# Performance work log

Hardware: AMD Instinct MI355X
Metric: run time of the kernel (lower is better)

The kernel has to match this reference:

```python
import jax, jax.numpy as jnp
import numpy as np

N_TRIALS, T, INPUT_DIM = 32, 512, 64
N, R, OUTPUT_DIM = 4096, 8, 64
DT = 0.1


def setup_inputs() -> dict:
    key = jax.random.key(0)
    k_inp, k_B, k_W, k_m, k_n = jax.random.split(key, 5)
    inp = jax.random.normal(k_inp, (N_TRIALS, T, INPUT_DIM), dtype=jnp.float32)
    B = jax.random.normal(k_B, (N, INPUT_DIM), dtype=jnp.float32)
    W = jax.random.normal(k_W, (OUTPUT_DIM, N), dtype=jnp.float32) / np.sqrt(N)
    m = jax.random.normal(k_m, (N, R), dtype=jnp.float32)
    n = jax.random.normal(k_n, (N, R), dtype=jnp.float32)
    return {"inp": inp, "B": B, "W": W, "m": m, "n": n}


def reference(inp, B, W, m, n):
    # inp: [b, t, i]; B: [N, i]; W: [o, N]; m, n: [N, r]
    n_trials = inp.shape[0]
    # Precompute input projection for all steps: [t, b, N]
    inp_proj = jnp.einsum('bti,ni->tbn', inp, B)

    def step(x, u):
        # x: [b, N] voltage; u: [b, N] projected input at this step
        # sigmoid(x) @ (m n^T / N)^T == ((sigmoid(x) @ n) @ m^T) / N
        rec = (jax.nn.sigmoid(x) @ n) @ m.T / N
        x_new = (1.0 - DT) * x + DT * (rec + u)
        y = jax.nn.sigmoid(x_new) @ W.T  # [b, o]
        return x_new, (x_new, y)

    x0 = jnp.zeros((n_trials, N), dtype=inp.dtype)
    _, (xs, ys) = jax.lax.scan(step, x0, inp_proj)
    # xs: [t, b, N]; ys: [t, b, o]
    x_seq = jnp.concatenate([x0[None], xs], axis=0).transpose(1, 0, 2)  # [b, t+1, N]
    output_seq = ys.transpose(1, 0, 2)  # [b, t, o]
    return (x_seq, output_seq)
```

## Files before the change

### kernel.cpp

```cpp
#include <hip/hip_runtime.h>

static constexpr int BTRIALS = 32;
static constexpr int TSTEPS  = 512;
static constexpr int IDIM    = 64;
static constexpr int NDIM    = 4096;
static constexpr int RDIM    = 8;
static constexpr int ODIM    = 64;

typedef short v8s __attribute__((ext_vector_type(8)));
typedef float v4f __attribute__((ext_vector_type(4)));

__device__ __forceinline__ float fast_sigmoid(float x) {
    float e = __builtin_amdgcn_exp2f(x * -1.44269504088896340736f);
    return __builtin_amdgcn_rcpf(1.0f + e);
}

template <int CTRL, int RMASK>
__device__ __forceinline__ float dpp_add(float v) {
    int moved = __builtin_amdgcn_update_dpp(0, __float_as_int(v), CTRL, RMASK, 0xf, true);
    return v + __int_as_float(moved);
}

__device__ __forceinline__ float wave_reduce_to_lane63(float v) {
    v = dpp_add<0x111, 0xf>(v);
    v = dpp_add<0x112, 0xf>(v);
    v = dpp_add<0x114, 0xf>(v);
    v = dpp_add<0x118, 0xf>(v);
    v = dpp_add<0x142, 0xa>(v);
    v = dpp_add<0x143, 0xc>(v);
    return v;
}

__device__ __forceinline__ short f2bf(float f) {
    unsigned u = __float_as_uint(f);
    u += 0x7FFFu + ((u >> 16) & 1u);
    return (short)(u >> 16);
}

__global__ __launch_bounds__(256) void split_conv(const float* __restrict__ src,
                                                  unsigned short* __restrict__ hi,
                                                  unsigned short* __restrict__ lo,
                                                  float scale) {
    const int base = (blockIdx.x * 256 + threadIdx.x) * 8;
    float4 a = *(const float4*)(src + base);
    float4 b = *(const float4*)(src + base + 4);
    float v[8] = {a.x, a.y, a.z, a.w, b.x, b.y, b.z, b.w};
    v8s h, l;
    #pragma unroll
    for (int j = 0; j < 8; ++j) {
        float f  = v[j] * scale;
        short hb = f2bf(f);
        h[j] = hb;
        float fh = __uint_as_float(((unsigned)(unsigned short)hb) << 16);
        l[j] = f2bf(f - fh);
    }
    *(v8s*)(hi + base) = h;
    *(v8s*)(lo + base) = l;
}

__global__ __launch_bounds__(256) void wconv(const float* __restrict__ W,
                                             unsigned short* __restrict__ Wb) {
    const int base = (blockIdx.x * 256 + threadIdx.x) * 8;
    float4 a = *(const float4*)(W + base);
    float4 b = *(const float4*)(W + base + 4);
    v8s o;
    o[0] = f2bf(a.x); o[1] = f2bf(a.y); o[2] = f2bf(a.z); o[3] = f2bf(a.w);
    o[4] = f2bf(b.x); o[5] = f2bf(b.y); o[6] = f2bf(b.z); o[7] = f2bf(b.w);
    *(v8s*)(Wb + base) = o;
}

__global__ __launch_bounds__(256) void pre_gemm_mfma(const unsigned short* __restrict__ Ah,
                                                     const unsigned short* __restrict__ Al,
                                                     const unsigned short* __restrict__ Bh,
                                                     const unsigned short* __restrict__ Bl,
                                                     float* __restrict__ u, int t0) {
    const int tid  = threadIdx.x;
    const int lane = tid & 63;
    const int wv   = tid >> 6;
    const int lm   = lane & 15;
    const int kq   = lane >> 4;

    const int mloc = blockIdx.x * 16 + lm;
    const int b    = mloc & 31;
    const int t    = t0 + (mloc >> 5);
    const size_t arow = (size_t)b * TSTEPS + t;

    const unsigned short* pah = Ah + arow * IDIM + kq * 8;
    const unsigned short* pal = Al + arow * IDIM + kq * 8;
    v8s ah0 = *(const v8s*)(pah);
    v8s ah1 = *(const v8s*)(pah + 32);
    v8s al0 = *(const v8s*)(pal);
    v8s al1 = *(const v8s*)(pal + 32);

    const int n0   = wv * 1024;
    const int urow = blockIdx.x * 16 + kq * 4;

    #pragma unroll 2
    for (int nt = 0; nt < 64; ++nt) {
        const int n = n0 + nt * 16 + lm;
        const unsigned short* pbh = Bh + (size_t)n * IDIM + kq * 8;
        const unsigned short* pbl = Bl + (size_t)n * IDIM + kq * 8;
        v8s bh0 = *(const v8s*)(pbh);
        v8s bh1 = *(const v8s*)(pbh + 32);
        v8s bl0 = *(const v8s*)(pbl);
        v8s bl1 = *(const v8s*)(pbl + 32);
        v4f acc = (v4f){0.f, 0.f, 0.f, 0.f};
        acc = __builtin_amdgcn_mfma_f32_16x16x32_bf16(ah0, bl0, acc, 0, 0, 0);
        acc = __builtin_amdgcn_mfma_f32_16x16x32_bf16(al0, bh0, acc, 0, 0, 0);
        acc = __builtin_amdgcn_mfma_f32_16x16x32_bf16(ah1, bl1, acc, 0, 0, 0);
        acc = __builtin_amdgcn_mfma_f32_16x16x32_bf16(al1, bh1, acc, 0, 0, 0);
        acc = __builtin_amdgcn_mfma_f32_16x16x32_bf16(ah0, bh0, acc, 0, 0, 0);
        acc = __builtin_amdgcn_mfma_f32_16x16x32_bf16(ah1, bh1, acc, 0, 0, 0);
        float* up = u + (size_t)urow * NDIM + n0 + nt * 16 + lm;
        #pragma unroll
        for (int r = 0; r < 4; ++r) up[(size_t)r * NDIM] = acc[r];
    }
}

__global__ __launch_bounds__(512, 2) void scan_kernel(const float* __restrict__ mmat,
                                                      const float* __restrict__ nmat,
                                                      const float* __restrict__ u,
                                                      float* __restrict__ xseq,
                                                      float* __restrict__ xstate,
                                                      unsigned short* __restrict__ sbuf,
                                                      int t0, int tc) {
    const int b    = blockIdx.x;
    const int tid  = threadIdx.x;
    const int j0   = tid * 8;
    const int lane = tid & 63;
    const int wv   = tid >> 6;

    __shared__ __align__(16) float wlds[2][64];

    float nm[8][8], mmr[8][8], x[8], s[8];
    const float4* np4 = (const float4*)(nmat + (size_t)j0 * RDIM);
    const float4* mp4 = (const float4*)(mmat + (size_t)j0 * RDIM);
    const float mscale = 0.1f / 4096.0f;
    #pragma unroll
    for (int j = 0; j < 8; ++j) {
        float4 a = np4[j * 2], c = np4[j * 2 + 1];
        nm[j][0] = a.x; nm[j][1] = a.y; nm[j][2] = a.z; nm[j][3] = a.w;
        nm[j][4] = c.x; nm[j][5] = c.y; nm[j][6] = c.z; nm[j][7] = c.w;
        float4 d = mp4[j * 2], e = mp4[j * 2 + 1];
        mmr[j][0] = d.x * mscale; mmr[j][1] = d.y * mscale;
        mmr[j][2] = d.z * mscale; mmr[j][3] = d.w * mscale;
        mmr[j][4] = e.x * mscale; mmr[j][5] = e.y * mscale;
        mmr[j][6] = e.z * mscale; mmr[j][7] = e.w * mscale;
    }

    if (t0 == 0) {
        #pragma unroll
        for (int j = 0; j < 8; ++j) x[j] = 0.0f;
        float* z = xseq + (size_t)b * (TSTEPS + 1) * NDIM + j0;
        *(float4*)(z + 0) = make_float4(0.f, 0.f, 0.f, 0.f);
        *(float4*)(z + 4) = make_float4(0.f, 0.f, 0.f, 0.f);
    } else {
        const float* xs = xstate + (size_t)b * NDIM + j0;
        float4 v0 = *(const float4*)(xs + 0);
        float4 v1 = *(const float4*)(xs + 4);
        x[0] = v0.x; x[1] = v0.y; x[2] = v0.z; x[3] = v0.w;
        x[4] = v1.x; x[5] = v1.y; x[6] = v1.z; x[7] = v1.w;
    }
    #pragma unroll
    for (int j = 0; j < 8; ++j) s[j] = fast_sigmoid(x[j]);

    float uv[8];
    {
        const float* up = u + ((size_t)0 * BTRIALS + b) * NDIM + j0;
        float4 v0 = *(const float4*)(up + 0);
        float4 v1 = *(const float4*)(up + 4);
        uv[0] = v0.x; uv[1] = v0.y; uv[2] = v0.z; uv[3] = v0.w;
        uv[4] = v1.x; uv[5] = v1.y; uv[6] = v1.z; uv[7] = v1.w;
    }

    for (int tl = 0; tl < tc; ++tl) {
        const int buf = tl & 1;
        const int tn = (tl + 1 < tc) ? (tl + 1) : tl;
        const float* upn = u + ((size_t)tn * BTRIALS + b) * NDIM + j0;
        float4 pf0 = *(const float4*)(upn + 0);
        float4 pf1 = *(const float4*)(upn + 4);

        float part[8];
        #pragma unroll
        for (int r = 0; r < 8; ++r) part[r] = 0.0f;
        #pragma unroll
        for (int j = 0; j < 8; ++j) {
            #pragma unroll
            for (int r = 0; r < 8; ++r) part[r] = fmaf(s[j], nm[j][r], part[r]);
        }
        #pragma unroll
        for (int r = 0; r < 8; ++r) part[r] = wave_reduce_to_lane63(part[r]);

        if (lane == 63) {
            #pragma unroll
            for (int r = 0; r < 8; ++r) wlds[buf][r * 8 + wv] = part[r];
        }

        float xd[8];
        #pragma unroll
        for (int j = 0; j < 8; ++j) xd[j] = fmaf(0.9f, x[j], uv[j]);

        __syncthreads();

        float v = wlds[buf][lane];
        v = dpp_add<0x111, 0xf>(v);
        v = dpp_add<0x112, 0xf>(v);
        v = dpp_add<0x114, 0xf>(v);

        float ps[8];
        #pragma unroll
        for (int r = 0; r < 8; ++r)
            ps[r] = __int_as_float(__builtin_amdgcn_readlane(__float_as_int(v), r * 8 + 7));

        float* xrow = xseq + ((size_t)b * (TSTEPS + 1) + (t0 + tl + 1)) * NDIM + j0;
        #pragma unroll
        for (int j = 0; j < 8; ++j) {
            float acc = xd[j];
            #pragma unroll
            for (int r = 0; r < 8; ++r) acc = fmaf(ps[r], mmr[j][r], acc);
            x[j] = acc;
        }
        *(float4*)(xrow + 0) = make_float4(x[0], x[1], x[2], x[3]);
        *(float4*)(xrow + 4) = make_float4(x[4], x[5], x[6], x[7]);

        #pragma unroll
        for (int j = 0; j < 8; ++j) s[j] = fast_sigmoid(x[j]);
        int c0, c1, c2, c3;
        asm("v_cvt_pk_bf16_f32 %0, %1, %2" : "=v"(c0) : "v"(s[0]), "v"(s[1]));
        asm("v_cvt_pk_bf16_f32 %0, %1, %2" : "=v"(c1) : "v"(s[2]), "v"(s[3]));
        asm("v_cvt_pk_bf16_f32 %0, %1, %2" : "=v"(c2) : "v"(s[4]), "v"(s[5]));
        asm("v_cvt_pk_bf16_f32 %0, %1, %2" : "=v"(c3) : "v"(s[6]), "v"(s[7]));
        *(int4*)((void*)(sbuf + ((size_t)b * tc + tl) * NDIM + j0)) = make_int4(c0, c1, c2, c3);

        uv[0] = pf0.x; uv[1] = pf0.y; uv[2] = pf0.z; uv[3] = pf0.w;
        uv[4] = pf1.x; uv[5] = pf1.y; uv[6] = pf1.z; uv[7] = pf1.w;
    }

    float* xs = xstate + (size_t)b * NDIM + j0;
    *(float4*)(xs + 0) = make_float4(x[0], x[1], x[2], x[3]);
    *(float4*)(xs + 4) = make_float4(x[4], x[5], x[6], x[7]);
}

__global__ __launch_bounds__(256) void y_gemm(const unsigned short* __restrict__ sbuf,
                                              const unsigned short* __restrict__ Wb,
                                              float* __restrict__ yout,
                                              int t0, int tc) {
    const int tid  = threadIdx.x;
    const int lane = tid & 63;
    const int mt   = blockIdx.x * 4 + (tid >> 6);
    const int lm   = lane & 15;
    const int kq   = lane >> 4;

    const int tilesPerB = tc >> 4;
    const int b  = mt / tilesPerB;
    const int tt = mt % tilesPerB;

    const unsigned short* pa = sbuf + ((size_t)b * tc + tt * 16 + lm) * NDIM + kq * 8;
    const unsigned short* pw = Wb + (size_t)lm * NDIM + kq * 8;

    v4f acc[4];
    #pragma unroll
    for (int ot = 0; ot < 4; ++ot) acc[ot] = (v4f){0.f, 0.f, 0.f, 0.f};

    #pragma unroll 4
    for (int kc = 0; kc < NDIM; kc += 32) {
        v8s af = *(const v8s*)(pa + kc);
        #pragma unroll
        for (int ot = 0; ot < 4; ++ot) {
            v8s bf = *(const v8s*)(pw + (size_t)ot * 16 * NDIM + kc);
            acc[ot] = __builtin_amdgcn_mfma_f32_16x16x32_bf16(af, bf, acc[ot], 0, 0, 0);
        }
    }

    #pragma unroll
    for (int ot = 0; ot < 4; ++ot) {
        #pragma unroll
        for (int r = 0; r < 4; ++r) {
            const int row = b * TSTEPS + t0 + tt * 16 + kq * 4 + r;
            yout[(size_t)row * ODIM + ot * 16 + lm] = acc[ot][r];
        }
    }
}

extern "C" void kernel_launch(void* const* d_in, const int* in_sizes, int n_in,
                              void* d_out, int out_size, void* d_ws, size_t ws_size,
                              hipStream_t stream) {
    const float* inp = (const float*)d_in[0];
    const float* Bm  = (const float*)d_in[1];
    const float* Wm  = (const float*)d_in[2];
    const float* mm  = (const float*)d_in[3];
    const float* nm  = (const float*)d_in[4];

    float* out  = (float*)d_out;
    float* xseq = out;
    float* yout = out + (size_t)BTRIALS * (TSTEPS + 1) * NDIM;

    float* xstate      = (float*)d_ws;
    unsigned short* Wb = (unsigned short*)(xstate + (size_t)BTRIALS * NDIM);
    unsigned short* Ah = Wb + (size_t)ODIM * NDIM;
    unsigned short* Al = Ah + (size_t)BTRIALS * TSTEPS * IDIM;
    unsigned short* Bh = Al + (size_t)BTRIALS * TSTEPS * IDIM;
    unsigned short* Bl = Bh + (size_t)NDIM * IDIM;
    float* ubuf        = (float*)(Bl + (size_t)NDIM * IDIM);

    const size_t head = (size_t)((char*)ubuf - (char*)d_ws);
    const size_t perstep = (size_t)BTRIALS * NDIM * (sizeof(float) + sizeof(unsigned short));
    size_t avail = (ws_size > head) ? (ws_size - head) : 0;
    int Tc = (int)(avail / perstep);
    if (Tc > TSTEPS) Tc = TSTEPS;
    Tc &= ~15;
    if (Tc < 16) Tc = 16;

    wconv<<<(ODIM * NDIM) / (256 * 8), 256, 0, stream>>>(Wm, Wb);
    split_conv<<<(BTRIALS * TSTEPS * IDIM) / (256 * 8), 256, 0, stream>>>(inp, Ah, Al, 0.1f);
    split_conv<<<(NDIM * IDIM) / (256 * 8), 256, 0, stream>>>(Bm, Bh, Bl, 1.0f);

    for (int t0 = 0; t0 < TSTEPS; t0 += Tc) {
        const int tc = (TSTEPS - t0 < Tc) ? (TSTEPS - t0) : Tc;
        unsigned short* sbuf = (unsigned short*)(ubuf + (size_t)tc * BTRIALS * NDIM);
        const int rows = tc * BTRIALS;
        pre_gemm_mfma<<<rows / 16, 256, 0, stream>>>(Ah, Al, Bh, Bl, ubuf, t0);
        scan_kernel<<<BTRIALS, 512, 0, stream>>>(mm, nm, ubuf, xseq, xstate, sbuf, t0, tc);
        const int mtiles = BTRIALS * (tc / 16);
        y_gemm<<<mtiles / 4, 256, 0, stream>>>(sbuf, Wb, yout, t0, tc);
    }
}
```

Before: 1.070 ms.

## Split scan into serial rank-8 recurrence and parallel state replay kernel

The serial scan kernel no longer writes the full x sequence or the bf16 sigmoid buffer each step. It records only the 8 reduced rank coefficients per step in a small buffer. A new x_replay kernel, launched on more blocks, rebuilds x, writes x_seq and the bf16 sigmoids in parallel across the trial and N dimensions. The u prefetch in the scan is also deepened to two steps ahead. This moves the large memory writes off the 32-block serial critical path, at the cost of an extra launch and reading u twice.

```diff
diff --git a/kernel.cpp b/kernel.cpp
--- a/kernel.cpp
+++ b/kernel.cpp
@@ -120,9 +120,8 @@
 __global__ __launch_bounds__(512, 2) void scan_kernel(const float* __restrict__ mmat,
                                                       const float* __restrict__ nmat,
                                                       const float* __restrict__ u,
-                                                      float* __restrict__ xseq,
                                                       float* __restrict__ xstate,
-                                                      unsigned short* __restrict__ sbuf,
+                                                      float* __restrict__ psbuf,
                                                       int t0, int tc) {
     const int b    = blockIdx.x;
     const int tid  = threadIdx.x;
@@ -151,9 +150,6 @@
     if (t0 == 0) {
         #pragma unroll
         for (int j = 0; j < 8; ++j) x[j] = 0.0f;
-        float* z = xseq + (size_t)b * (TSTEPS + 1) * NDIM + j0;
-        *(float4*)(z + 0) = make_float4(0.f, 0.f, 0.f, 0.f);
-        *(float4*)(z + 4) = make_float4(0.f, 0.f, 0.f, 0.f);
     } else {
         const float* xs = xstate + (size_t)b * NDIM + j0;
         float4 v0 = *(const float4*)(xs + 0);
@@ -172,13 +168,17 @@
         uv[0] = v0.x; uv[1] = v0.y; uv[2] = v0.z; uv[3] = v0.w;
         uv[4] = v1.x; uv[5] = v1.y; uv[6] = v1.z; uv[7] = v1.w;
     }
+    const int t1 = (1 < tc) ? 1 : tc - 1;
+    const int t2 = (2 < tc) ? 2 : tc - 1;
+    const float* up1 = u + ((size_t)t1 * BTRIALS + b) * NDIM + j0;
+    const float* up2 = u + ((size_t)t2 * BTRIALS + b) * NDIM + j0;
+    float4 p0a = *(const float4*)(up1 + 0);
+    float4 p0b = *(const float4*)(up1 + 4);
+    float4 p1a = *(const float4*)(up2 + 0);
+    float4 p1b = *(const float4*)(up2 + 4);
 
     for (int tl = 0; tl < tc; ++tl) {
         const int buf = tl & 1;
-        const int tn = (tl + 1 < tc) ? (tl + 1) : tl;
-        const float* upn = u + ((size_t)tn * BTRIALS + b) * NDIM + j0;
-        float4 pf0 = *(const float4*)(upn + 0);
-        float4 pf1 = *(const float4*)(upn + 4);
 
         float part[8];
         #pragma unroll
@@ -212,7 +212,12 @@
         for (int r = 0; r < 8; ++r)
             ps[r] = __int_as_float(__builtin_amdgcn_readlane(__float_as_int(v), r * 8 + 7));
 
-        float* xrow = xseq + ((size_t)b * (TSTEPS + 1) + (t0 + tl + 1)) * NDIM + j0;
+        if (tid == 0) {
+            float* pp = psbuf + ((size_t)b * TSTEPS + (t0 + tl)) * 8;
+            *(float4*)(pp + 0) = make_float4(ps[0], ps[1], ps[2], ps[3]);
+            *(float4*)(pp + 4) = make_float4(ps[4], ps[5], ps[6], ps[7]);
+        }
+
         #pragma unroll
         for (int j = 0; j < 8; ++j) {
             float acc = xd[j];
@@ -220,25 +225,94 @@
             for (int r = 0; r < 8; ++r) acc = fmaf(ps[r], mmr[j][r], acc);
             x[j] = acc;
         }
-        *(float4*)(xrow + 0) = make_float4(x[0], x[1], x[2], x[3]);
-        *(float4*)(xrow + 4) = make_float4(x[4], x[5], x[6], x[7]);
-
         #pragma unroll
         for (int j = 0; j < 8; ++j) s[j] = fast_sigmoid(x[j]);
-        int c0, c1, c2, c3;
-        asm("v_cvt_pk_bf16_f32 %0, %1, %2" : "=v"(c0) : "v"(s[0]), "v"(s[1]));
-        asm("v_cvt_pk_bf16_f32 %0, %1, %2" : "=v"(c1) : "v"(s[2]), "v"(s[3]));
-        asm("v_cvt_pk_bf16_f32 %0, %1, %2" : "=v"(c2) : "v"(s[4]), "v"(s[5]));
-        asm("v_cvt_pk_bf16_f32 %0, %1, %2" : "=v"(c3) : "v"(s[6]), "v"(s[7]));
-        *(int4*)((void*)(sbuf + ((size_t)b * tc + tl) * NDIM + j0)) = make_int4(c0, c1, c2, c3);
-
-        uv[0] = pf0.x; uv[1] = pf0.y; uv[2] = pf0.z; uv[3] = pf0.w;
-        uv[4] = pf1.x; uv[5] = pf1.y; uv[6] = pf1.z; uv[7] = pf1.w;
+
+        uv[0] = p0a.x; uv[1] = p0a.y; uv[2] = p0a.z; uv[3] = p0a.w;
+        uv[4] = p0b.x; uv[5] = p0b.y; uv[6] = p0b.z; uv[7] = p0b.w;
+        p0a = p1a; p0b = p1b;
+        const int tn = (tl + 3 < tc) ? (tl + 3) : (tc - 1);
+        const float* upn = u + ((size_t)tn * BTRIALS + b) * NDIM + j0;
+        p1a = *(const float4*)(upn + 0);
+        p1b = *(const float4*)(upn + 4);
     }
 
     float* xs = xstate + (size_t)b * NDIM + j0;
     *(float4*)(xs + 0) = make_float4(x[0], x[1], x[2], x[3]);
     *(float4*)(xs + 4) = make_float4(x[4], x[5], x[6], x[7]);
+}
+
+__global__ __launch_bounds__(256) void x_replay(const float* __restrict__ mmat,
+                                                const float* __restrict__ u,
+                                                const float* __restrict__ psbuf,
+                                                float* __restrict__ xseq,
+                                                unsigned short* __restrict__ sbuf,
+                                                int t0, int tc) {
+    const int tid = threadIdx.x;
+    const int b   = blockIdx.y;
+    const int n0  = blockIdx.x * 512 + tid * 2;
+
+    const float mscale = 0.1f / 4096.0f;
+    float mm0[8], mm1[8];
+    {
+        float4 d0 = *(const float4*)(mmat + (size_t)n0 * RDIM);
+        float4 d1 = *(const float4*)(mmat + (size_t)n0 * RDIM + 4);
+        float4 e0 = *(const float4*)(mmat + (size_t)(n0 + 1) * RDIM);
+        float4 e1 = *(const float4*)(mmat + (size_t)(n0 + 1) * RDIM + 4);
+        mm0[0] = d0.x * mscale; mm0[1] = d0.y * mscale; mm0[2] = d0.z * mscale; mm0[3] = d0.w * mscale;
+        mm0[4] = d1.x * mscale; mm0[5] = d1.y * mscale; mm0[6] = d1.z * mscale; mm0[7] = d1.w * mscale;
+        mm1[0] = e0.x * mscale; mm1[1] = e0.y * mscale; mm1[2] = e0.z * mscale; mm1[3] = e0.w * mscale;
+        mm1[4] = e1.x * mscale; mm1[5] = e1.y * mscale; mm1[6] = e1.z * mscale; mm1[7] = e1.w * mscale;
+    }
+
+    float x0, x1;
+    if (t0 == 0) {
+        x0 = 0.f; x1 = 0.f;
+        *(float2*)(xseq + (size_t)b * (TSTEPS + 1) * NDIM + n0) = make_float2(0.f, 0.f);
+    } else {
+        float2 v = *(const float2*)(xseq + ((size_t)b * (TSTEPS + 1) + t0) * NDIM + n0);
+        x0 = v.x; x1 = v.y;
+    }
+
+    const int t1 = (1 < tc) ? 1 : tc - 1;
+    const int t2 = (2 < tc) ? 2 : tc - 1;
+    float2 uv = *(const float2*)(u + ((size_t)0 * BTRIALS + b) * NDIM + n0);
+    float2 q0 = *(const float2*)(u + ((size_t)t1 * BTRIALS + b) * NDIM + n0);
+    float2 q1 = *(const float2*)(u + ((size_t)t2 * BTRIALS + b) * NDIM + n0);
+    const float* pp0 = psbuf + ((size_t)b * TSTEPS + t0) * 8;
+    float4 psa = *(const float4*)(pp0 + 0);
+    float4 psb = *(const float4*)(pp0 + 4);
+
+    for (int tl = 0; tl < tc; ++tl) {
+        float ps[8] = {psa.x, psa.y, psa.z, psa.w, psb.x, psb.y, psb.z, psb.w};
+
+        const int tpn = (tl + 1 < tc) ? (tl + 1) : tl;
+        const float* ppn = psbuf + ((size_t)b * TSTEPS + (t0 + tpn)) * 8;
+        float4 npa = *(const float4*)(ppn + 0);
+        float4 npb = *(const float4*)(ppn + 4);
+
+        float xd0 = fmaf(0.9f, x0, uv.x);
+        float xd1 = fmaf(0.9f, x1, uv.y);
+        #pragma unroll
+        for (int r = 0; r < 8; ++r) xd0 = fmaf(ps[r], mm0[r], xd0);
+        #pragma unroll
+        for (int r = 0; r < 8; ++r) xd1 = fmaf(ps[r], mm1[r], xd1);
+        x0 = xd0; x1 = xd1;
+
+        *(float2*)(xseq + ((size_t)b * (TSTEPS + 1) + (t0 + tl + 1)) * NDIM + n0) =
+            make_float2(x0, x1);
+
+        float s0 = fast_sigmoid(x0);
+        float s1 = fast_sigmoid(x1);
+        int c;
+        asm("v_cvt_pk_bf16_f32 %0, %1, %2" : "=v"(c) : "v"(s0), "v"(s1));
+        *(int*)((void*)(sbuf + ((size_t)b * tc + tl) * NDIM + n0)) = c;
+
+        uv = q0; q0 = q1;
+        const int tn = (tl + 3 < tc) ? (tl + 3) : (tc - 1);
+        q1 = *(const float2*)(u + ((size_t)tn * BTRIALS + b) * NDIM + n0);
+        psa = npa; psb = npb;
+    }
 }
 
 __global__ __launch_bounds__(256) void y_gemm(const unsigned short* __restrict__ sbuf,
@@ -301,7 +375,8 @@
     unsigned short* Al = Ah + (size_t)BTRIALS * TSTEPS * IDIM;
     unsigned short* Bh = Al + (size_t)BTRIALS * TSTEPS * IDIM;
     unsigned short* Bl = Bh + (size_t)NDIM * IDIM;
-    float* ubuf        = (float*)(Bl + (size_t)NDIM * IDIM);
+    float* psbuf       = (float*)(Bl + (size_t)NDIM * IDIM);
+    float* ubuf        = psbuf + (size_t)BTRIALS * TSTEPS * RDIM;
 
     const size_t head = (size_t)((char*)ubuf - (char*)d_ws);
     const size_t perstep = (size_t)BTRIALS * NDIM * (sizeof(float) + sizeof(unsigned short));
@@ -320,7 +395,8 @@
         unsigned short* sbuf = (unsigned short*)(ubuf + (size_t)tc * BTRIALS * NDIM);
         const int rows = tc * BTRIALS;
         pre_gemm_mfma<<<rows / 16, 256, 0, stream>>>(Ah, Al, Bh, Bl, ubuf, t0);
-        scan_kernel<<<BTRIALS, 512, 0, stream>>>(mm, nm, ubuf, xseq, xstate, sbuf, t0, tc);
+        scan_kernel<<<BTRIALS, 512, 0, stream>>>(mm, nm, ubuf, xstate, psbuf, t0, tc);
+        x_replay<<<dim3(8, BTRIALS), 256, 0, stream>>>(mm, ubuf, psbuf, xseq, sbuf, t0, tc);
         const int mtiles = BTRIALS * (tc / 16);
         y_gemm<<<mtiles / 4, 256, 0, stream>>>(sbuf, Wb, yout, t0, tc);
     }
```

Measured after the change: 1.296 ms. 1.21x slower.
